# Performance work log

Measured on AMD Instinct MI355X. Metric: run time of the kernel, lower is better.

## Reference

```python
import jax, jax.numpy as jnp
import numpy as np

B, N, S = 8, 16384, 2048
C1, C2 = 128, 256
MLP = [256, 256]
BN_EPS = 1e-5


def setup_inputs() -> dict:
    key = jax.random.key(0)
    ks = jax.random.split(key, 12)
    inp = {
        "xyz1": jax.random.normal(ks[0], (B, N, 3), dtype=jnp.float32),
        "xyz2": jax.random.normal(ks[1], (B, S, 3), dtype=jnp.float32),
        "points1": jax.random.normal(ks[2], (B, C1, N), dtype=jnp.float32),
        "points2": jax.random.normal(ks[3], (B, C2, S), dtype=jnp.float32),
    }
    cin = C1 + C2
    kidx = 4
    for li, cout in enumerate(MLP):
        inp[f"W{li}"] = jax.random.normal(ks[kidx], (cout, cin), dtype=jnp.float32) * (1.0 / np.sqrt(cin))
        inp[f"b{li}"] = jnp.zeros((cout,), dtype=jnp.float32)
        inp[f"g{li}"] = jnp.ones((cout,), dtype=jnp.float32)
        inp[f"beta{li}"] = jnp.zeros((cout,), dtype=jnp.float32)
        cin = cout
        kidx += 1
    return inp


def _interpolate(xyz1, xyz2, points2):
    # D[b,n,s] = ||xyz1[b,n] - xyz2[b,s]||^2
    D = jnp.sum((xyz1[:, :, None, :] - xyz2[:, None, :, :]) ** 2, axis=-1)  # [B,N,S]
    neg_dist, idx = jax.lax.top_k(-D, 3)  # 3 smallest distances, ascending
    dist = jnp.maximum(-neg_dist, 1e-10)  # [B,N,3]
    w = 1.0 / dist
    weight = w / jnp.sum(w, axis=2, keepdims=True)  # [B,N,3]
    p2 = jnp.transpose(points2, (0, 2, 1))  # [B,S,C2]
    gathered = p2[jnp.arange(p2.shape[0])[:, None, None], idx]  # [B,N,3,C2]
    return jnp.einsum("bnkc,bnk->bcn", gathered, weight)  # [B,C2,N]


def _conv_bn_relu(x, W, b, g, beta):
    # 1x1 conv over points: [B,Cin,N] -> [B,Cout,N]
    y = jnp.einsum("oc,bcn->bon", W, x) + b[None, :, None]
    mean = jnp.mean(y, axis=(0, 2), keepdims=True)
    var = jnp.var(y, axis=(0, 2), keepdims=True)  # biased, training-mode BN
    yh = (y - mean) * jax.lax.rsqrt(var + BN_EPS)
    return jax.nn.relu(yh * g[None, :, None] + beta[None, :, None])


def reference(xyz1, xyz2, points1, points2, W0, b0, g0, beta0, W1, b1, g1, beta1):
    interp = _interpolate(xyz1, xyz2, points2)  # [B,C2,N]
    h = jnp.concatenate([interp, points1], axis=1)  # [B,C1+C2,N]
    h = _conv_bn_relu(h, W0, b0, g0, beta0)
    h = _conv_bn_relu(h, W1, b1, g1, beta1)
    return h
```

## Files before the change

kernel.cpp:

```cpp
#include <hip/hip_runtime.h>
#include <hip/hip_bf16.h>


typedef unsigned int u32;
typedef unsigned short u16;
typedef unsigned long long u64;
typedef __attribute__((ext_vector_type(8))) short short8;
typedef __attribute__((ext_vector_type(4))) float f32x4;

#define NT_TOTAL 131072
#define NN 16384
#define SS 2048

__device__ __forceinline__ float bf2f(u16 u) {
    union { u32 i; float f; } cv; cv.i = ((u32)u) << 16; return cv.f;
}
__device__ __forceinline__ u16 f2bf(float f) {
    union { float f; u32 i; } cv; cv.f = f;
    const u32 r = (cv.i + 0x7FFFu + ((cv.i >> 16) & 1u)) >> 16;
    return (u16)r;
}
__device__ __forceinline__ float ldf(const void* p, int i, int isbf) {
    return isbf ? bf2f(((const u16*)p)[i]) : ((const float*)p)[i];
}

__global__ __launch_bounds__(256)
void detect_kernel(const u32* __restrict__ xyz1w, u32* __restrict__ flag,
                   float* __restrict__ stats)
{
    __shared__ int cnt;
    const int t = threadIdx.x;
    if (t == 0) cnt = 0;
    for (int i = t; i < 1024; i += 256) stats[i] = 0.f;
    __syncthreads();
    if (t < 64) {
        const u32 w = xyz1w[t];
        const int e = (int)((w >> 7) & 0xFF);
        if (e >= 96 && e <= 144) atomicAdd(&cnt, 1);
    }
    __syncthreads();
    if (t == 0) flag[0] = (cnt >= 48) ? 1u : 0u;
}

__global__ __launch_bounds__(256)
void sentinel_kernel(u16* __restrict__ out, int n)
{
    const int i = blockIdx.x * 256 + threadIdx.x;
    if (i < n) out[i] = 0x4496;
}

__global__ __launch_bounds__(256)
void param_kernel(const void* W0, const void* b0, const void* g0, const void* bt0,
                  const void* W1, const void* b1, const void* g1, const void* bt1,
                  const u32* __restrict__ flag,
                  u16* __restrict__ Wb0, u16* __restrict__ Wb1, float* __restrict__ pf)
{
    const int isbf = (int)flag[0];
    const int i = blockIdx.x * 256 + threadIdx.x;
    if (i < 98304) Wb0[i] = f2bf(ldf(W0, i, isbf));
    if (i < 65536) Wb1[i] = f2bf(ldf(W1, i, isbf));
    if (i < 1536) {
        const void* srcs[6] = { b0, g0, bt0, b1, g1, bt1 };
        pf[i] = ldf(srcs[i >> 8], i & 255, isbf);
    }
}

__global__ __launch_bounds__(256)
void pack2_kernel(const void* __restrict__ xyz2, float4* __restrict__ s2q,
                  const u32* __restrict__ flag)
{
    const int isbf = (int)flag[0];
    const int i = blockIdx.x * 256 + threadIdx.x;
    if (i < 8 * SS) {
        const float x = ldf(xyz2, i * 3 + 0, isbf);
        const float y = ldf(xyz2, i * 3 + 1, isbf);
        const float z = ldf(xyz2, i * 3 + 2, isbf);
        float4 v; v.x = x; v.y = y; v.z = z; v.w = x * x + y * y + z * z;
        s2q[i] = v;
    }
}

__global__ __launch_bounds__(256)
void transpose_kernel(const void* __restrict__ in, u16* __restrict__ out,
                      int Cc, int Np, int ldout, int coff, const u32* __restrict__ flag)
{
    __shared__ u16 tile[64][72];
    const int isbf = (int)flag[0];
    const int t = threadIdx.x;
    const int n0 = blockIdx.x * 64, c0 = blockIdx.y * 64, bz = blockIdx.z;
    const int ch = t & 7, r = t >> 3;
#pragma unroll
    for (int p = 0; p < 2; ++p) {
        const int cl = r + p * 32;
        const size_t idx = ((size_t)(bz * Cc + c0 + cl)) * Np + n0 + ch * 8;
        union { uint4 v; u16 us[8]; } pk;
        if (isbf) {
            pk.v = *(const uint4*)((const u16*)in + idx);
        } else {
            const float4 va = *(const float4*)((const float*)in + idx);
            const float4 vb = *(const float4*)((const float*)in + idx + 4);
            pk.us[0] = f2bf(va.x); pk.us[1] = f2bf(va.y);
            pk.us[2] = f2bf(va.z); pk.us[3] = f2bf(va.w);
            pk.us[4] = f2bf(vb.x); pk.us[5] = f2bf(vb.y);
            pk.us[6] = f2bf(vb.z); pk.us[7] = f2bf(vb.w);
        }
        *(uint4*)&tile[cl][ch * 8] = pk.v;
    }
    __syncthreads();
#pragma unroll
    for (int p = 0; p < 2; ++p) {
        const int nl = r + p * 32;
        union { uint4 v; u16 us[8]; } pk;
#pragma unroll
        for (int i = 0; i < 8; ++i) pk.us[i] = tile[ch * 8 + i][nl];
        *(uint4*)&out[((size_t)(bz * Np + n0 + nl)) * ldout + coff + c0 + ch * 8] = pk.v;
    }
}

__global__ __launch_bounds__(256)
void knn_kernel(const float4* __restrict__ s2q, const void* __restrict__ xyz1,
                u32* __restrict__ idxA, float* __restrict__ wA,
                const u32* __restrict__ flag)
{
    __shared__ float skeys[4][64][5];
    const int isbf = (int)flag[0];
    const int t = threadIdx.x;
    const int lane = t & 63;
    const int wid = __builtin_amdgcn_readfirstlane(t >> 6);
    const int qg = blockIdx.x * 64 + lane;
    const int b = blockIdx.x >> 8;
    const float qx = ldf(xyz1, qg * 3 + 0, isbf);
    const float qy = ldf(xyz1, qg * 3 + 1, isbf);
    const float qz = ldf(xyz1, qg * 3 + 2, isbf);
    const float qx2 = -2.f * qx, qy2 = -2.f * qy, qz2 = -2.f * qz;
    const float qc = qx * qx + qy * qy + qz * qz;
    const float4* __restrict__ S = s2q + (size_t)b * SS;

    float k0 = __builtin_inff(), k1 = k0, k2 = k0, k3 = k0, k4 = k0;
    const int sbase = wid * 512;
#pragma unroll 8
    for (int it = 0; it < 512; ++it) {
        const int s = sbase + it;
        const float4 v = S[s];
        float d = fmaf(v.x, qx2, qc);
        d = fmaf(v.y, qy2, d);
        d = fmaf(v.z, qz2, d);
        d += v.w;
        const float k = __uint_as_float((__float_as_uint(d) & 0xFFFFF800u) | (u32)s);
        const float o0 = fminf(k, k0);
        const float o1 = __builtin_amdgcn_fmed3f(k, k0, k1);
        const float o2 = __builtin_amdgcn_fmed3f(k, k1, k2);
        const float o3 = __builtin_amdgcn_fmed3f(k, k2, k3);
        const float o4 = __builtin_amdgcn_fmed3f(k, k3, k4);
        k0 = o0; k1 = o1; k2 = o2; k3 = o3; k4 = o4;
    }
    skeys[wid][lane][0] = k0;
    skeys[wid][lane][1] = k1;
    skeys[wid][lane][2] = k2;
    skeys[wid][lane][3] = k3;
    skeys[wid][lane][4] = k4;
    __syncthreads();
    if (wid != 0) return;

    u64 e0 = ~0ull, e1 = ~0ull, e2 = ~0ull;
#pragma unroll
    for (int w = 0; w < 4; ++w)
#pragma unroll
        for (int i = 0; i < 5; ++i) {
            const u32 idx = __float_as_uint(skeys[w][lane][i]) & 0x7FFu;
            const float4 c = S[idx];
            const float dx = qx - c.x, dy = qy - c.y, dz = qz - c.z;
            const float d = fmaf(dz, dz, fmaf(dy, dy, dx * dx));
            const u64 e = ((u64)__float_as_uint(d) << 11) | (u64)idx;
            const bool c0 = e < e0, c1 = e < e1, c2 = e < e2;
            e2 = c1 ? e1 : (c2 ? e : e2);
            e1 = c0 ? e0 : (c1 ? e : e1);
            e0 = c0 ? e : e0;
        }
    const u32 i0 = (u32)(e0 & 0x7FF), i1 = (u32)(e1 & 0x7FF), i2 = (u32)(e2 & 0x7FF);
    const float d0 = fmaxf(__uint_as_float((u32)(e0 >> 11)), 1e-10f);
    const float d1 = fmaxf(__uint_as_float((u32)(e1 >> 11)), 1e-10f);
    const float d2 = fmaxf(__uint_as_float((u32)(e2 >> 11)), 1e-10f);
    const float w0 = 1.f / d0, w1 = 1.f / d1, w2 = 1.f / d2;
    const float inv = 1.f / (w0 + w1 + w2);
    idxA[qg * 3 + 0] = i0; idxA[qg * 3 + 1] = i1; idxA[qg * 3 + 2] = i2;
    wA[qg * 3 + 0] = w0 * inv; wA[qg * 3 + 1] = w1 * inv; wA[qg * 3 + 2] = w2 * inv;
}

__global__ __launch_bounds__(256)
void interp_kernel(const u16* __restrict__ p2T, const u32* __restrict__ idxA,
                   const float* __restrict__ wA, u16* __restrict__ hT)
{
    const int t = threadIdx.x;
    const int pl = t >> 5, g = t & 31;
    const int qg = blockIdx.x * 8 + pl;
    const int b = qg >> 14;
    float acc[8] = {0.f, 0.f, 0.f, 0.f, 0.f, 0.f, 0.f, 0.f};
#pragma unroll
    for (int k = 0; k < 3; ++k) {
        const u32 idx = idxA[qg * 3 + k];
        const float w = wA[qg * 3 + k];
        union { uint4 v; u16 us[8]; } pk;
        pk.v = *(const uint4*)(p2T + ((size_t)(b * SS + idx)) * 256 + g * 8);
#pragma unroll
        for (int e = 0; e < 8; ++e) acc[e] = fmaf(w, bf2f(pk.us[e]), acc[e]);
    }
    union { uint4 v; u16 us[8]; } ov;
#pragma unroll
    for (int e = 0; e < 8; ++e) ov.us[e] = f2bf(acc[e]);
    *(uint4*)&hT[(size_t)qg * 384 + g * 8] = ov.v;
}

#define GEMM_BODY(BUF, OTH, KCUR)                                                        \
    {                                                                                    \
        short8 a[4], b[4];                                                               \
        _Pragma("unroll")                                                                \
        for (int i = 0; i < 4; ++i) a[i] = *(const short8*)&aT[BUF][aoff[i]];            \
        _Pragma("unroll")                                                                \
        for (int j = 0; j < 4; ++j) b[j] = *(const short8*)&bT[BUF][boff[j]];            \
        _Pragma("unroll")                                                                \
        for (int i = 0; i < 4; ++i)                                                      \
            _Pragma("unroll")                                                            \
            for (int j = 0; j < 4; ++j)                                                  \
                acc[i][j] = __builtin_amdgcn_mfma_f32_16x16x32_bf16(a[i], b[j], acc[i][j], 0, 0, 0); \
        if ((KCUR) + 32 < K) {                                                           \
            *(uint4*)&aT[OTH][o0] = ra0; *(uint4*)&aT[OTH][o1] = ra1;                    \
            *(uint4*)&bT[OTH][o0] = rb0; *(uint4*)&bT[OTH][o1] = rb1;                    \
            if ((KCUR) + 64 < K) {                                                       \
                ra0 = *(const uint4*)(gA0 + (KCUR) + 64);                                \
                ra1 = *(const uint4*)(gA1 + (KCUR) + 64);                                \
                rb0 = *(const uint4*)(gB0 + (KCUR) + 64);                                \
                rb1 = *(const uint4*)(gB1 + (KCUR) + 64);                                \
            }                                                                            \
        }                                                                                \
        __syncthreads();                                                                 \
    }

__global__ __launch_bounds__(256)
void gemm_kernel(const u16* __restrict__ A, const u16* __restrict__ Bm,
                 const float* __restrict__ bias, void* __restrict__ yout, int K,
                 const u32* __restrict__ flag,
                 float* __restrict__ sums, float* __restrict__ sumsq, int outmode)
{
    __shared__ __align__(16) u16 lds[18432];
    u16* const aT[2] = { lds, lds + 4096 };
    u16* const bT[2] = { lds + 8192, lds + 12288 };
    float* const sds = (float*)(lds + 17408);

    const int isbf = (int)flag[0];
    const int t = threadIdx.x;
    const int lane = t & 63;
    const int l15 = lane & 15;
    const int q = lane >> 4;
    const int wid = t >> 6;
    const int n0 = blockIdx.x * 128;
    const int m0 = blockIdx.y * 128;
    const int wm = (wid & 1) * 64;
    const int wn = (wid >> 1) * 64;
    const int wp = wid >> 1;

    f32x4 acc[4][4] = {};

    const int ca0 = t, ca1 = t + 256;
    const u16* gA0 = A + (size_t)(m0 + (ca0 >> 2)) * K + (ca0 & 3) * 8;
    const u16* gA1 = A + (size_t)(m0 + (ca1 >> 2)) * K + (ca1 & 3) * 8;
    const u16* gB0 = Bm + (size_t)(n0 + (ca0 >> 2)) * K + (ca0 & 3) * 8;
    const u16* gB1 = Bm + (size_t)(n0 + (ca1 >> 2)) * K + (ca1 & 3) * 8;
    const int o0 = (ca0 >> 2) * 32 + (((ca0 & 3) ^ ((ca0 >> 3) & 3)) * 8);
    const int o1 = (ca1 >> 2) * 32 + (((ca1 & 3) ^ ((ca1 >> 3) & 3)) * 8);

    const int gsw = (l15 >> 1) & 3;
    int aoff[4], boff[4];
#pragma unroll
    for (int i = 0; i < 4; ++i) {
        aoff[i] = (wm + i * 16 + l15) * 32 + ((q ^ gsw) * 8);
        boff[i] = (wn + i * 16 + l15) * 32 + ((q ^ gsw) * 8);
    }

    uint4 ra0 = *(const uint4*)(gA0);
    uint4 ra1 = *(const uint4*)(gA1);
    uint4 rb0 = *(const uint4*)(gB0);
    uint4 rb1 = *(const uint4*)(gB1);
    *(uint4*)&aT[0][o0] = ra0; *(uint4*)&aT[0][o1] = ra1;
    *(uint4*)&bT[0][o0] = rb0; *(uint4*)&bT[0][o1] = rb1;
    ra0 = *(const uint4*)(gA0 + 32);
    ra1 = *(const uint4*)(gA1 + 32);
    rb0 = *(const uint4*)(gB0 + 32);
    rb1 = *(const uint4*)(gB1 + 32);
    __syncthreads();

    for (int kk = 0; kk < K; kk += 64) {
        GEMM_BODY(0, 1, kk)
        GEMM_BODY(1, 0, kk + 32)
    }

    if (outmode) {
#pragma unroll
        for (int i = 0; i < 4; ++i) {
            const int mloc = wm + i * 16 + q * 4;
            float bi[4];
#pragma unroll
            for (int r = 0; r < 4; ++r) bi[r] = bias[m0 + mloc + r];
#pragma unroll
            for (int r = 0; r < 4; ++r) {
                float s = 0.f, sq = 0.f;
#pragma unroll
                for (int j = 0; j < 4; ++j) {
                    const float v = acc[i][j][r] + bi[r];
                    s += v; sq += v * v;
                }
#pragma unroll
                for (int off = 1; off < 16; off <<= 1) {
                    s += __shfl_xor(s, off);
                    sq += __shfl_xor(sq, off);
                }
                if (l15 == 0) {
                    sds[wp * 128 + mloc + r] = s;
                    sds[256 + wp * 128 + mloc + r] = sq;
                }
            }
#pragma unroll
            for (int j = 0; j < 4; ++j) {
                const int nl = wn + j * 16 + l15;
                union { u64 w; u16 us[4]; } pk;
#pragma unroll
                for (int r = 0; r < 4; ++r) pk.us[r] = f2bf(acc[i][j][r] + bi[r]);
                *(u64*)&lds[nl * 136 + mloc] = pk.w;
            }
        }
        __syncthreads();
        u16* outp = (u16*)yout;
#pragma unroll
        for (int it = 0; it < 8; ++it) {
            const int row = (t >> 4) + it * 16;
            const int cc = (t & 15) * 8;
            const uint4 v = *(const uint4*)&lds[row * 136 + cc];
            *(uint4*)&outp[((size_t)(n0 + row)) * 256 + m0 + cc] = v;
        }
        if (t < 128) {
            atomicAdd(&sums[m0 + t], sds[t] + sds[128 + t]);
        } else if (t < 256) {
            const int c = t - 128;
            atomicAdd(&sumsq[m0 + c], sds[256 + c] + sds[384 + c]);
        }
        return;
    }

#pragma unroll
    for (int i = 0; i < 4; ++i) {
        const int mBase = m0 + wm + i * 16 + q * 4;
        float bi[4];
#pragma unroll
        for (int r = 0; r < 4; ++r) bi[r] = bias[mBase + r];
#pragma unroll
        for (int j = 0; j < 4; ++j) {
            const int col = n0 + wn + j * 16 + l15;
            const size_t obase = ((size_t)(col >> 14) * 256) * NN + (col & 16383);
#pragma unroll
            for (int r = 0; r < 4; ++r) {
                const float v = acc[i][j][r] + bi[r];
                const size_t oi = obase + (size_t)(mBase + r) * NN;
                if (isbf) ((u16*)yout)[oi] = f2bf(v);
                else      ((float*)yout)[oi] = v;
            }
        }
    }
#pragma unroll
    for (int i = 0; i < 4; ++i) {
        const int mloc = wm + i * 16 + q * 4;
#pragma unroll
        for (int r = 0; r < 4; ++r) {
            const float bi = bias[m0 + mloc + r];
            float s = 0.f, sq = 0.f;
#pragma unroll
            for (int j = 0; j < 4; ++j) {
                const float v = acc[i][j][r] + bi;
                s += v; sq += v * v;
            }
#pragma unroll
            for (int off = 1; off < 16; off <<= 1) {
                s += __shfl_xor(s, off);
                sq += __shfl_xor(sq, off);
            }
            if (l15 == 0) {
                sds[wp * 128 + mloc + r] = s;
                sds[256 + wp * 128 + mloc + r] = sq;
            }
        }
    }
    __syncthreads();
    if (t < 128) {
        atomicAdd(&sums[m0 + t], sds[t] + sds[128 + t]);
    } else if (t < 256) {
        const int c = t - 128;
        atomicAdd(&sumsq[m0 + c], sds[256 + c] + sds[384 + c]);
    }
}

__global__ __launch_bounds__(256)
void bn_elem_kernel(const u16* __restrict__ h0, const float* __restrict__ sums,
                    const float* __restrict__ sumsq, const float* __restrict__ gam,
                    const float* __restrict__ beta, u16* __restrict__ h2)
{
    __shared__ float ssc[256], ssh[256];
    const int t = threadIdx.x;
    {
        const float invNT = 1.0f / (float)NT_TOTAL;
        const float mean = sums[t] * invNT;
        const float var = sumsq[t] * invNT - mean * mean;
        const float rstd = rsqrtf(var + 1e-5f);
        const float sc = gam[t] * rstd;
        ssc[t] = sc;
        ssh[t] = beta[t] - mean * sc;
    }
    __syncthreads();
    for (u32 g = blockIdx.x * 256 + t; g < 4194304u; g += 4096u * 256u) {
        const int cb = (g & 31) * 8;
        union { uint4 v; u16 us[8]; } iv, ov;
        iv.v = *(const uint4*)(h0 + (size_t)g * 8);
#pragma unroll
        for (int e = 0; e < 8; ++e) {
            float v = bf2f(iv.us[e]) * ssc[cb + e] + ssh[cb + e];
            v = (v != v) ? 777.0f : fmaxf(v, 0.f);
            ov.us[e] = f2bf(v);
        }
        *(uint4*)(h2 + (size_t)g * 8) = ov.v;
    }
}

__global__ __launch_bounds__(256)
void final_kernel(void* __restrict__ y, const float* __restrict__ sums,
                  const float* __restrict__ sumsq, const float* __restrict__ gam,
                  const float* __restrict__ beta, const u32* __restrict__ flag)
{
    const int isbf = (int)flag[0];
    const int gid = blockIdx.x * 256 + threadIdx.x;
    const int c = (gid >> 12) & 255;
    const float invNT = 1.0f / (float)NT_TOTAL;
    const float mean = sums[c] * invNT;
    const float var = sumsq[c] * invNT - mean * mean;
    const float rstd = rsqrtf(var + 1e-5f);
    const float sc = gam[c] * rstd;
    const float sh = beta[c] - mean * sc;
    const size_t idx4 = (size_t)gid * 4;
    float in4[4];
    if (isbf) {
        union { uint2 v2; u16 us[4]; } iv;
        iv.v2 = *(const uint2*)((const u16*)y + idx4);
#pragma unroll
        for (int e = 0; e < 4; ++e) in4[e] = bf2f(iv.us[e]);
    } else {
        const float4 v = *(const float4*)((const float*)y + idx4);
        in4[0] = v.x; in4[1] = v.y; in4[2] = v.z; in4[3] = v.w;
    }
    float o4[4];
#pragma unroll
    for (int e = 0; e < 4; ++e) {
        float v = in4[e] * sc + sh;
        o4[e] = (v != v) ? 777.0f : fmaxf(v, 0.f);
    }
    if (isbf) {
        union { uint2 v2; u16 us[4]; } o;
#pragma unroll
        for (int e = 0; e < 4; ++e) o.us[e] = f2bf(o4[e]);
        *(uint2*)((u16*)y + idx4) = o.v2;
    } else {
        float4 o; o.x = o4[0]; o.y = o4[1]; o.z = o4[2]; o.w = o4[3];
        *(float4*)((float*)y + idx4) = o;
    }
}

__global__ void pointnet_fp_module_24532853195517_kernel() {}

extern "C" void kernel_launch(void* const* d_in, const int* in_sizes, int n_in,
                              void* d_out, int out_size, void* d_ws, size_t ws_size,
                              hipStream_t stream)
{
    const void* xyz1    = d_in[0];
    const void* xyz2    = d_in[1];
    const void* points1 = d_in[2];
    const void* points2 = d_in[3];
    const void* W0 = d_in[4];  const void* b0 = d_in[5];
    const void* g0 = d_in[6];  const void* bt0 = d_in[7];
    const void* W1 = d_in[8];  const void* b1 = d_in[9];
    const void* g1 = d_in[10]; const void* bt1 = d_in[11];

    char* ws = (char*)d_ws;
    float* stats = (float*)ws;
    u32* flag    = (u32*)(ws + 4096);
    float* pf    = (float*)(ws + 8192);
    u16* Wb0     = (u16*)(ws + 16384);
    u16* Wb1     = (u16*)(ws + 212992);
    u32* idxA    = (u32*)(ws + 344064);
    float* wA    = (float*)(ws + 1916928);
    u16* p2T     = (u16*)(ws + 3489792);
    u16* hT      = (u16*)(ws + 11878400);
    u16* h2      = hT;
    float* sum0 = stats, *sq0 = stats + 256, *sum1 = stats + 512, *sq1 = stats + 768;

    u16* h0 = (u16*)d_out;
    float4* s2q = (float4*)((char*)d_out + (8u << 20));

    if (ws_size < (size_t)112541696) {
        sentinel_kernel<<<(out_size + 255) / 256, 256, 0, stream>>>((u16*)d_out, out_size);
        return;
    }

    sentinel_kernel<<<16, 256, 0, stream>>>((u16*)d_out, 4096);

    detect_kernel<<<1, 256, 0, stream>>>((const u32*)xyz1, flag, stats);
    param_kernel<<<384, 256, 0, stream>>>(W0, b0, g0, bt0, W1, b1, g1, bt1, flag, Wb0, Wb1, pf);
    pack2_kernel<<<64, 256, 0, stream>>>(xyz2, s2q, flag);
    transpose_kernel<<<dim3(32, 4, 8), 256, 0, stream>>>(points2, p2T, 256, 2048, 256, 0, flag);
    transpose_kernel<<<dim3(256, 2, 8), 256, 0, stream>>>(points1, hT, 128, 16384, 384, 256, flag);
    knn_kernel<<<2048, 256, 0, stream>>>(s2q, xyz1, idxA, wA, flag);
    interp_kernel<<<16384, 256, 0, stream>>>(p2T, idxA, wA, hT);
    gemm_kernel<<<dim3(1024, 2), 256, 0, stream>>>(Wb0, hT, pf + 0, h0, 384, flag, sum0, sq0, 1);
    bn_elem_kernel<<<4096, 256, 0, stream>>>(h0, sum0, sq0, pf + 256, pf + 512, h2);
    gemm_kernel<<<dim3(1024, 2), 256, 0, stream>>>(Wb1, h2, pf + 768, d_out, 256, flag, sum1, sq1, 0);
    final_kernel<<<32768, 256, 0, stream>>>(d_out, sum1, sq1, pf + 1024, pf + 1280, flag);
}
```

Baseline: 534.4 us.

## Fuse BN-ReLU into second GEMM operand load and write GEMM0 output in place

The standalone batchnorm/ReLU elementwise kernel is removed. Its scale/shift is now applied to the B-operand tiles as the second GEMM loads them from global memory, which drops one full read/write pass over the intermediate activation. GEMM0 is restructured so each block covers all 256 output channels for 64 points and writes its result in place into the hT buffer it read from. Both GEMMs now load the weight (A) operand directly from global memory into registers instead of staging it through LDS. The risks are extra VALU work inside the GEMM loop, the in-place overwrite being safe only because each block reads and writes only its own rows, and the loss of the NaN-to-777 sentinel handling.

```diff
diff --git a/kernel.cpp b/kernel.cpp
--- a/kernel.cpp
+++ b/kernel.cpp
@@ -211,42 +211,160 @@
     *(uint4*)&hT[(size_t)qg * 384 + g * 8] = ov.v;
 }
 
-#define GEMM_BODY(BUF, OTH, KCUR)                                                        \
+#define K0 384
+#define G0_STEP(BUF, OTH, KCUR, RAC, RAN, RBW)                                           \
     {                                                                                    \
-        short8 a[4], b[4];                                                               \
-        _Pragma("unroll")                                                                \
-        for (int i = 0; i < 4; ++i) a[i] = *(const short8*)&aT[BUF][aoff[i]];            \
-        _Pragma("unroll")                                                                \
-        for (int j = 0; j < 4; ++j) b[j] = *(const short8*)&bT[BUF][boff[j]];            \
+        short8 a4[4], b4[4];                                                             \
+        _Pragma("unroll")                                                                \
+        for (int i = 0; i < 4; ++i) a4[i] = *(short8*)&RAC[i];                           \
+        _Pragma("unroll")                                                                \
+        for (int j = 0; j < 4; ++j)                                                      \
+            b4[j] = *(const short8*)&bT[BUF][(j * 16 + l15) * 32 + (q ^ gsw) * 8];       \
+        if ((KCUR) + 32 < K0) {                                                          \
+            _Pragma("unroll")                                                            \
+            for (int i = 0; i < 4; ++i)                                                  \
+                RAN[i] = *(const uint4*)(gA + i * 16 * K0 + (KCUR) + 32);                \
+        }                                                                                \
         _Pragma("unroll")                                                                \
         for (int i = 0; i < 4; ++i)                                                      \
             _Pragma("unroll")                                                            \
             for (int j = 0; j < 4; ++j)                                                  \
-                acc[i][j] = __builtin_amdgcn_mfma_f32_16x16x32_bf16(a[i], b[j], acc[i][j], 0, 0, 0); \
-        if ((KCUR) + 32 < K) {                                                           \
-            *(uint4*)&aT[OTH][o0] = ra0; *(uint4*)&aT[OTH][o1] = ra1;                    \
-            *(uint4*)&bT[OTH][o0] = rb0; *(uint4*)&bT[OTH][o1] = rb1;                    \
-            if ((KCUR) + 64 < K) {                                                       \
-                ra0 = *(const uint4*)(gA0 + (KCUR) + 64);                                \
-                ra1 = *(const uint4*)(gA1 + (KCUR) + 64);                                \
-                rb0 = *(const uint4*)(gB0 + (KCUR) + 64);                                \
-                rb1 = *(const uint4*)(gB1 + (KCUR) + 64);                                \
+                acc[i][j] = __builtin_amdgcn_mfma_f32_16x16x32_bf16(a4[i], b4[j], acc[i][j], 0, 0, 0); \
+        if ((KCUR) + 32 < K0) {                                                          \
+            *(uint4*)&bT[OTH][ob] = RBW;                                                 \
+            if ((KCUR) + 96 < K0) RBW = *(const uint4*)(gB + (KCUR) + 96);               \
+        }                                                                                \
+        __syncthreads();                                                                 \
+    }
+
+__global__ __launch_bounds__(256)
+void gemm0_kernel(const u16* __restrict__ A, u16* __restrict__ hTio,
+                  const float* __restrict__ bias,
+                  float* __restrict__ sums, float* __restrict__ sumsq)
+{
+    __shared__ __align__(16) u16 bT[2][64 * 32];
+    __shared__ float sds[512];
+    const int t = threadIdx.x;
+    const int lane = t & 63;
+    const int l15 = lane & 15;
+    const int q = lane >> 4;
+    const int wid = t >> 6;
+    const int n0 = blockIdx.x * 64;
+    const int wm = wid * 64;
+
+    f32x4 acc[4][4] = {};
+
+    const u16* gB = hTio + (size_t)(n0 + (t >> 2)) * 384 + (t & 3) * 8;
+    const int ob = (t >> 2) * 32 + (((t & 3) ^ ((t >> 3) & 3)) * 8);
+    const u16* gA = A + (size_t)(wm + l15) * K0 + q * 8;
+    const int gsw = (l15 >> 1) & 3;
+
+    uint4 raA[4], raB[4], rbA, rbB;
+    {
+        const uint4 r0 = *(const uint4*)gB;
+#pragma unroll
+        for (int i = 0; i < 4; ++i) raA[i] = *(const uint4*)(gA + i * 16 * K0);
+        *(uint4*)&bT[0][ob] = r0;
+        rbA = *(const uint4*)(gB + 32);
+        rbB = *(const uint4*)(gB + 64);
+        __syncthreads();
+    }
+
+#pragma unroll
+    for (int kk = 0; kk < K0; kk += 64) {
+        G0_STEP(0, 1, kk, raA, raB, rbA)
+        G0_STEP(1, 0, kk + 32, raB, raA, rbB)
+    }
+
+#pragma unroll
+    for (int i = 0; i < 4; ++i) {
+        const int mcb = wm + i * 16 + q * 4;
+        float bi4[4];
+#pragma unroll
+        for (int r = 0; r < 4; ++r) bi4[r] = bias[mcb + r];
+#pragma unroll
+        for (int j = 0; j < 4; ++j) {
+            const int nl = j * 16 + l15;
+            union { u64 w; u16 us[4]; } pk;
+#pragma unroll
+            for (int r = 0; r < 4; ++r) pk.us[r] = f2bf(acc[i][j][r] + bi4[r]);
+            *(u64*)&hTio[(size_t)(n0 + nl) * 384 + mcb] = pk.w;
+        }
+#pragma unroll
+        for (int r = 0; r < 4; ++r) {
+            float s = 0.f, sq = 0.f;
+#pragma unroll
+            for (int j = 0; j < 4; ++j) {
+                const float v = acc[i][j][r] + bi4[r];
+                s += v; sq += v * v;
+            }
+#pragma unroll
+            for (int off = 1; off < 16; off <<= 1) {
+                s += __shfl_xor(s, off);
+                sq += __shfl_xor(sq, off);
+            }
+            if (l15 == 0) { sds[mcb + r] = s; sds[256 + mcb + r] = sq; }
+        }
+    }
+    __syncthreads();
+    if (t < 256) {
+        atomicAdd(&sums[t], sds[t]);
+        atomicAdd(&sumsq[t], sds[256 + t]);
+    }
+}
+
+#define K1 256
+#define BNT(PKV, KB)                                                                     \
+    {                                                                                    \
+        _Pragma("unroll")                                                                \
+        for (int e = 0; e < 8; ++e) {                                                    \
+            const int kch = (KB) + kcofs + e;                                            \
+            float vv = bf2f(PKV.us[e]) * ssc[kch] + ssh[kch];                            \
+            PKV.us[e] = f2bf(fmaxf(vv, 0.f));                                            \
+        }                                                                                \
+    }
+#define G1_STEP(BUF, OTH, KCUR, RAC, RAN, RB0, RB1)                                      \
+    {                                                                                    \
+        short8 a4[4], b4[4];                                                             \
+        _Pragma("unroll")                                                                \
+        for (int i = 0; i < 4; ++i) a4[i] = *(short8*)&RAC[i];                           \
+        _Pragma("unroll")                                                                \
+        for (int j = 0; j < 4; ++j)                                                      \
+            b4[j] = *(const short8*)&bT[BUF][(wn + j * 16 + l15) * 32 + (q ^ gsw) * 8];  \
+        if ((KCUR) + 32 < K1) {                                                          \
+            _Pragma("unroll")                                                            \
+            for (int i = 0; i < 4; ++i)                                                  \
+                RAN[i] = *(const uint4*)(gA + i * 16 * K1 + (KCUR) + 32);                \
+        }                                                                                \
+        _Pragma("unroll")                                                                \
+        for (int i = 0; i < 4; ++i)                                                      \
+            _Pragma("unroll")                                                            \
+            for (int j = 0; j < 4; ++j)                                                  \
+                acc[i][j] = __builtin_amdgcn_mfma_f32_16x16x32_bf16(a4[i], b4[j], acc[i][j], 0, 0, 0); \
+        if ((KCUR) + 32 < K1) {                                                          \
+            BNT(RB0, (KCUR) + 32)                                                        \
+            BNT(RB1, (KCUR) + 32)                                                        \
+            *(uint4*)&bT[OTH][ob0] = RB0.v;                                              \
+            *(uint4*)&bT[OTH][ob1] = RB1.v;                                              \
+            if ((KCUR) + 96 < K1) {                                                      \
+                RB0.v = *(const uint4*)(gB0 + (KCUR) + 96);                              \
+                RB1.v = *(const uint4*)(gB1 + (KCUR) + 96);                              \
             }                                                                            \
         }                                                                                \
         __syncthreads();                                                                 \
     }
 
 __global__ __launch_bounds__(256)
-void gemm_kernel(const u16* __restrict__ A, const u16* __restrict__ Bm,
-                 const float* __restrict__ bias, void* __restrict__ yout, int K,
-                 const u32* __restrict__ flag,
-                 float* __restrict__ sums, float* __restrict__ sumsq, int outmode)
-{
-    __shared__ __align__(16) u16 lds[18432];
-    u16* const aT[2] = { lds, lds + 4096 };
-    u16* const bT[2] = { lds + 8192, lds + 12288 };
-    float* const sds = (float*)(lds + 17408);
-
+void gemm1_kernel(const u16* __restrict__ A, const u16* __restrict__ h0,
+                  const float* __restrict__ bias, void* __restrict__ yout,
+                  const u32* __restrict__ flag,
+                  float* __restrict__ sums, float* __restrict__ sumsq,
+                  const float* __restrict__ sum0, const float* __restrict__ sq0,
+                  const float* __restrict__ gam0, const float* __restrict__ beta0)
+{
+    __shared__ __align__(16) u16 bT[2][128 * 32];
+    __shared__ float sds[512];
+    __shared__ float ssc[256], ssh[256];
     const int isbf = (int)flag[0];
     const int t = threadIdx.x;
     const int lane = t & 63;
@@ -259,91 +377,51 @@
     const int wn = (wid >> 1) * 64;
     const int wp = wid >> 1;
 
+    {
+        const float invNT = 1.0f / (float)NT_TOTAL;
+        const float mean = sum0[t] * invNT;
+        const float var = sq0[t] * invNT - mean * mean;
+        const float rstd = rsqrtf(var + 1e-5f);
+        const float sc = gam0[t] * rstd;
+        ssc[t] = sc;
+        ssh[t] = beta0[t] - mean * sc;
+    }
+
     f32x4 acc[4][4] = {};
 
-    const int ca0 = t, ca1 = t + 256;
-    const u16* gA0 = A + (size_t)(m0 + (ca0 >> 2)) * K + (ca0 & 3) * 8;
-    const u16* gA1 = A + (size_t)(m0 + (ca1 >> 2)) * K + (ca1 & 3) * 8;
-    const u16* gB0 = Bm + (size_t)(n0 + (ca0 >> 2)) * K + (ca0 & 3) * 8;
-    const u16* gB1 = Bm + (size_t)(n0 + (ca1 >> 2)) * K + (ca1 & 3) * 8;
-    const int o0 = (ca0 >> 2) * 32 + (((ca0 & 3) ^ ((ca0 >> 3) & 3)) * 8);
-    const int o1 = (ca1 >> 2) * 32 + (((ca1 & 3) ^ ((ca1 >> 3) & 3)) * 8);
-
+    const u16* gB0 = h0 + (size_t)(n0 + (t >> 2)) * 384 + (t & 3) * 8;
+    const u16* gB1 = h0 + (size_t)(n0 + 64 + (t >> 2)) * 384 + (t & 3) * 8;
+    const int kcofs = (t & 3) * 8;
+    const int ob0 = (t >> 2) * 32 + (((t & 3) ^ ((t >> 3) & 3)) * 8);
+    const int ob1 = (64 + (t >> 2)) * 32 + (((t & 3) ^ ((t >> 3) & 3)) * 8);
+    const u16* gA = A + (size_t)(m0 + wm + l15) * K1 + q * 8;
     const int gsw = (l15 >> 1) & 3;
-    int aoff[4], boff[4];
-#pragma unroll
-    for (int i = 0; i < 4; ++i) {
-        aoff[i] = (wm + i * 16 + l15) * 32 + ((q ^ gsw) * 8);
-        boff[i] = (wn + i * 16 + l15) * 32 + ((q ^ gsw) * 8);
-    }
-
-    uint4 ra0 = *(const uint4*)(gA0);
-    uint4 ra1 = *(const uint4*)(gA1);
-    uint4 rb0 = *(const uint4*)(gB0);
-    uint4 rb1 = *(const uint4*)(gB1);
-    *(uint4*)&aT[0][o0] = ra0; *(uint4*)&aT[0][o1] = ra1;
-    *(uint4*)&bT[0][o0] = rb0; *(uint4*)&bT[0][o1] = rb1;
-    ra0 = *(const uint4*)(gA0 + 32);
-    ra1 = *(const uint4*)(gA1 + 32);
-    rb0 = *(const uint4*)(gB0 + 32);
-    rb1 = *(const uint4*)(gB1 + 32);
-    __syncthreads();
-
-    for (int kk = 0; kk < K; kk += 64) {
-        GEMM_BODY(0, 1, kk)
-        GEMM_BODY(1, 0, kk + 32)
-    }
-
-    if (outmode) {
-#pragma unroll
-        for (int i = 0; i < 4; ++i) {
-            const int mloc = wm + i * 16 + q * 4;
-            float bi[4];
-#pragma unroll
-            for (int r = 0; r < 4; ++r) bi[r] = bias[m0 + mloc + r];
-#pragma unroll
-            for (int r = 0; r < 4; ++r) {
-                float s = 0.f, sq = 0.f;
-#pragma unroll
-                for (int j = 0; j < 4; ++j) {
-                    const float v = acc[i][j][r] + bi[r];
-                    s += v; sq += v * v;
-                }
-#pragma unroll
-                for (int off = 1; off < 16; off <<= 1) {
-                    s += __shfl_xor(s, off);
-                    sq += __shfl_xor(sq, off);
-                }
-                if (l15 == 0) {
-                    sds[wp * 128 + mloc + r] = s;
-                    sds[256 + wp * 128 + mloc + r] = sq;
-                }
-            }
-#pragma unroll
-            for (int j = 0; j < 4; ++j) {
-                const int nl = wn + j * 16 + l15;
-                union { u64 w; u16 us[4]; } pk;
-#pragma unroll
-                for (int r = 0; r < 4; ++r) pk.us[r] = f2bf(acc[i][j][r] + bi[r]);
-                *(u64*)&lds[nl * 136 + mloc] = pk.w;
-            }
-        }
+
+    union PK { uint4 v; u16 us[8]; };
+    uint4 raA[4], raB[4];
+    PK rb0A, rb1A, rb0B, rb1B;
+    {
+        PK r0, r1;
+        r0.v = *(const uint4*)gB0;
+        r1.v = *(const uint4*)gB1;
+#pragma unroll
+        for (int i = 0; i < 4; ++i) raA[i] = *(const uint4*)(gA + i * 16 * K1);
         __syncthreads();
-        u16* outp = (u16*)yout;
-#pragma unroll
-        for (int it = 0; it < 8; ++it) {
-            const int row = (t >> 4) + it * 16;
-            const int cc = (t & 15) * 8;
-            const uint4 v = *(const uint4*)&lds[row * 136 + cc];
-            *(uint4*)&outp[((size_t)(n0 + row)) * 256 + m0 + cc] = v;
-        }
-        if (t < 128) {
-            atomicAdd(&sums[m0 + t], sds[t] + sds[128 + t]);
-        } else if (t < 256) {
-            const int c = t - 128;
-            atomicAdd(&sumsq[m0 + c], sds[256 + c] + sds[384 + c]);
-        }
-        return;
+        BNT(r0, 0)
+        BNT(r1, 0)
+        *(uint4*)&bT[0][ob0] = r0.v;
+        *(uint4*)&bT[0][ob1] = r1.v;
+        rb0A.v = *(const uint4*)(gB0 + 32);
+        rb1A.v = *(const uint4*)(gB1 + 32);
+        rb0B.v = *(const uint4*)(gB0 + 64);
+        rb1B.v = *(const uint4*)(gB1 + 64);
+        __syncthreads();
+    }
+
+#pragma unroll
+    for (int kk = 0; kk < K1; kk += 64) {
+        G1_STEP(0, 1, kk, raA, raB, rb0A, rb1A)
+        G1_STEP(1, 0, kk + 32, raB, raA, rb0B, rb1B)
     }
 
 #pragma unroll
@@ -394,37 +472,6 @@
     } else if (t < 256) {
         const int c = t - 128;
         atomicAdd(&sumsq[m0 + c], sds[256 + c] + sds[384 + c]);
-    }
-}
-
-__global__ __launch_bounds__(256)
-void bn_elem_kernel(const u16* __restrict__ h0, const float* __restrict__ sums,
-                    const float* __restrict__ sumsq, const float* __restrict__ gam,
-                    const float* __restrict__ beta, u16* __restrict__ h2)
-{
-    __shared__ float ssc[256], ssh[256];
-    const int t = threadIdx.x;
-    {
-        const float invNT = 1.0f / (float)NT_TOTAL;
-        const float mean = sums[t] * invNT;
-        const float var = sumsq[t] * invNT - mean * mean;
-        const float rstd = rsqrtf(var + 1e-5f);
-        const float sc = gam[t] * rstd;
-        ssc[t] = sc;
-        ssh[t] = beta[t] - mean * sc;
-    }
-    __syncthreads();
-    for (u32 g = blockIdx.x * 256 + t; g < 4194304u; g += 4096u * 256u) {
-        const int cb = (g & 31) * 8;
-        union { uint4 v; u16 us[8]; } iv, ov;
-        iv.v = *(const uint4*)(h0 + (size_t)g * 8);
-#pragma unroll
-        for (int e = 0; e < 8; ++e) {
-            float v = bf2f(iv.us[e]) * ssc[cb + e] + ssh[cb + e];
-            v = (v != v) ? 777.0f : fmaxf(v, 0.f);
-            ov.us[e] = f2bf(v);
-        }
-        *(uint4*)(h2 + (size_t)g * 8) = ov.v;
     }
 }
 
@@ -495,10 +542,8 @@
     float* wA    = (float*)(ws + 1916928);
     u16* p2T     = (u16*)(ws + 3489792);
     u16* hT      = (u16*)(ws + 11878400);
-    u16* h2      = hT;
     float* sum0 = stats, *sq0 = stats + 256, *sum1 = stats + 512, *sq1 = stats + 768;
 
-    u16* h0 = (u16*)d_out;
     float4* s2q = (float4*)((char*)d_out + (8u << 20));
 
     if (ws_size < (size_t)112541696) {
@@ -515,8 +560,8 @@
     transpose_kernel<<<dim3(256, 2, 8), 256, 0, stream>>>(points1, hT, 128, 16384, 384, 256, flag);
     knn_kernel<<<2048, 256, 0, stream>>>(s2q, xyz1, idxA, wA, flag);
     interp_kernel<<<16384, 256, 0, stream>>>(p2T, idxA, wA, hT);
-    gemm_kernel<<<dim3(1024, 2), 256, 0, stream>>>(Wb0, hT, pf + 0, h0, 384, flag, sum0, sq0, 1);
-    bn_elem_kernel<<<4096, 256, 0, stream>>>(h0, sum0, sq0, pf + 256, pf + 512, h2);
-    gemm_kernel<<<dim3(1024, 2), 256, 0, stream>>>(Wb1, h2, pf + 768, d_out, 256, flag, sum1, sq1, 0);
+    gemm0_kernel<<<2048, 256, 0, stream>>>(Wb0, hT, pf + 0, sum0, sq0);
+    gemm1_kernel<<<dim3(1024, 2), 256, 0, stream>>>(Wb1, hT, pf + 768, d_out, flag,
+                                                    sum1, sq1, sum0, sq0, pf + 256, pf + 512);
     final_kernel<<<32768, 256, 0, stream>>>(d_out, sum1, sq1, pf + 1024, pf + 1280, flag);
 }
```

Result: faster. 523.5 us (-2.0%).
